# Performance work log

Hardware: AMD Instinct MI355X
Metric: run time of the kernel (lower is better)

## Reference

```python
import jax, jax.numpy as jnp
import numpy as np

N, E, L, D, H = 20000, 100000, 4, 64, 8
HID = H * D  # LSTM hidden size = num_heads * out_dim


def setup_inputs() -> dict:
    key = jax.random.key(0)
    ks = jax.random.split(key, 8)
    s = 0.05
    return {
        "features": jax.random.normal(ks[0], (N, D), jnp.float32),
        "type_mask": jax.random.randint(ks[1], (N,), 0, 3),
        "edge_metapath_indices": jax.random.randint(ks[2], (E, L), 0, N),
        "dst": jax.random.randint(ks[3], (E,), 0, N),
        "W_ih": jax.random.normal(ks[4], (4 * HID, D), jnp.float32) * s,
        "W_hh": jax.random.normal(ks[5], (4 * HID, HID), jnp.float32) * s,
        "b_ih": jnp.zeros((4 * HID,), jnp.float32),
        "b_hh": jnp.zeros((4 * HID,), jnp.float32),
        "attn1_w": jax.random.normal(ks[6], (H, D), jnp.float32) * s,
        "attn2": jax.random.normal(ks[7], (1, H, D), jnp.float32) * s,
    }


def _lstm_last_hidden(x, W_ih, W_hh, b_ih, b_hh):
    # x: [L, E, D] time-major. PyTorch LSTM gate order: i, f, g, o.
    h0 = jnp.zeros((x.shape[1], W_hh.shape[1]), x.dtype)
    b = b_ih + b_hh

    def step(carry, xt):
        h, c = carry
        gates = xt @ W_ih.T + h @ W_hh.T + b  # [E, 4*HID]
        i, f, g, o = jnp.split(gates, 4, axis=-1)
        c = jax.nn.sigmoid(f) * c + jax.nn.sigmoid(i) * jnp.tanh(g)
        h = jax.nn.sigmoid(o) * jnp.tanh(c)
        return (h, c), None

    (h, _), _ = jax.lax.scan(step, (h0, h0), x)
    return h  # [E, HID]


def reference(features, type_mask, edge_metapath_indices, dst,
              W_ih, W_hh, b_ih, b_hh, attn1_w, attn2):
    alpha = 0.01  # LeakyReLU slope
    # gather metapath node features: [E, L, D]
    edata = features[edge_metapath_indices]
    h = _lstm_last_hidden(jnp.swapaxes(edata, 0, 1), W_ih, W_hh, b_ih, b_hh)
    eft = h.reshape(-1, H, D)  # [E, H, D]
    center = features[edge_metapath_indices[:, -1]]  # [E, D]
    a1 = center @ attn1_w.T                      # [E, H]
    a2 = jnp.sum(eft * attn2, axis=-1)           # [E, H]
    a = jax.nn.leaky_relu(a1 + a2, negative_slope=alpha)[:, :, None]  # [E, H, 1]
    # edge softmax: segmented by destination node
    amax = jax.ops.segment_max(a, dst, num_segments=N)
    amax = jnp.where(jnp.isfinite(amax), amax, 0.0)
    ex = jnp.exp(a - amax[dst])
    denom = jax.ops.segment_sum(ex, dst, num_segments=N)
    attn = ex / denom[dst]  # every edge's segment is nonempty
    # message passing: scatter-sum of eft * attn into dst nodes
    return jax.ops.segment_sum(eft * attn, dst, num_segments=N)  # [N, H, D]
```

## Files before the change

kernel.cpp:

```cpp
#include <hip/hip_runtime.h>
#include <hip/hip_bf16.h>
#include <stdint.h>

#define N_NODES 20000
#define E_EDGES 100000
#define L_SEQ   4
#define D_FEAT  64
#define H_HEADS 8
#define HID     512

typedef __attribute__((ext_vector_type(8))) short short8;
typedef __attribute__((ext_vector_type(4))) float floatx4;

__device__ __forceinline__ float sigmoidf_(float x) { return 1.0f / (1.0f + __expf(-x)); }
__device__ __forceinline__ float tanhf_(float x) {
    x = fminf(15.f, fmaxf(-15.f, x));
    float e = __expf(2.f * x);
    return (e - 1.f) / (e + 1.f);
}
__device__ __forceinline__ unsigned fkey(float f) {
    unsigned u = __float_as_uint(f);
    return (u & 0x80000000u) ? ~u : (u | 0x80000000u);
}
__device__ __forceinline__ float fdecode(unsigned k) {
    if (k == 0u) return 0.0f;
    unsigned u = (k & 0x80000000u) ? (k ^ 0x80000000u) : ~k;
    return __uint_as_float(u);
}
__device__ __forceinline__ short f2bf(float x) {
    __hip_bfloat16 b = __float2bfloat16(x);
    return *(short*)&b;
}
__device__ __forceinline__ float bf2f(short x) {
    __hip_bfloat16 b = *(__hip_bfloat16*)&x;
    return __bfloat162float(b);
}

__device__ __forceinline__ void gload16(const void* g, const void* l) {
    __builtin_amdgcn_global_load_lds(
        (const __attribute__((address_space(1))) unsigned int*)(uintptr_t)g,
        (__attribute__((address_space(3))) unsigned int*)(unsigned int)(uintptr_t)l,
        16, 0, 0);
}

__global__ __launch_bounds__(256) void feat2bf16(const float* __restrict__ f, short* __restrict__ fb) {
    int i = blockIdx.x * 256 + threadIdx.x;
    if (i < N_NODES * D_FEAT) fb[i] = f2bf(f[i]);
}

__global__ __launch_bounds__(128) void convert_weights(
    const float* __restrict__ W_ih, const float* __restrict__ W_hh,
    const float* __restrict__ b_ih, const float* __restrict__ b_hh,
    short* __restrict__ Wb_ih, short* __restrict__ Wb_hh, float* __restrict__ bias)
{
    int rp = blockIdx.x;
    int hblock = rp >> 7, rem = rp & 127;
    int half = (rem >> 6) & 1, gate = (rem >> 4) & 3, j = rem & 15;
    int ro = gate * HID + hblock * 32 + half * 16 + j;
    for (int k = threadIdx.x; k < D_FEAT; k += 128)
        Wb_ih[rp * D_FEAT + k] = f2bf(W_ih[ro * D_FEAT + k]);
    for (int k = threadIdx.x; k < HID; k += 128)
        Wb_hh[rp * HID + k] = f2bf(W_hh[ro * HID + k]);
    if (threadIdx.x == 0) bias[ro] = b_ih[ro] + b_hh[ro];
}

__global__ __launch_bounds__(256) void deg_hist(const int* __restrict__ dst, int* __restrict__ deg) {
    int i = blockIdx.x * 256 + threadIdx.x;
    if (i < E_EDGES) atomicAdd(&deg[dst[i]], 1);
}

__global__ __launch_bounds__(1024) void scan_deg(const int* __restrict__ deg,
                                                 int* __restrict__ row, int* __restrict__ cursor) {
    __shared__ int buf[1024];
    __shared__ int s_carry;
    const int tid = threadIdx.x;
    if (tid == 0) s_carry = 0;
    __syncthreads();
    for (int base = 0; base < N_NODES; base += 1024) {
        int idx = base + tid;
        int v = (idx < N_NODES) ? deg[idx] : 0;
        buf[tid] = v;
        __syncthreads();
        for (int offd = 1; offd < 1024; offd <<= 1) {
            int tv = (tid >= offd) ? buf[tid - offd] : 0;
            __syncthreads();
            buf[tid] += tv;
            __syncthreads();
        }
        int c0 = s_carry;
        if (idx < N_NODES) { row[idx] = c0 + buf[tid] - v; cursor[idx] = c0 + buf[tid] - v; }
        __syncthreads();
        if (tid == 1023) s_carry = c0 + buf[1023];
        __syncthreads();
    }
    if (tid == 0) row[N_NODES] = s_carry;
}

__global__ __launch_bounds__(256) void fill_csr(const int* __restrict__ dst,
                                                int* __restrict__ cursor, int* __restrict__ elist) {
    int i = blockIdx.x * 256 + threadIdx.x;
    if (i < E_EDGES) {
        int p = atomicAdd(&cursor[dst[i]], 1);
        elist[p] = i;
    }
}

template <int FIRST>
__global__ __launch_bounds__(256) void lstm_mfma(
    const short* __restrict__ feats_bf,
    const int*   __restrict__ mp,
    const short* __restrict__ Wb_ih,
    const short* __restrict__ Wb_hh,
    const float* __restrict__ bias,
    const short* __restrict__ h_prev,
    short*       __restrict__ h_next,
    short*       __restrict__ c_state,
    int t, int cnt, int nslices)
{
    __shared__ __align__(16) short At[128 * 64];
    __shared__ __align__(16) short Bt[128 * 64];

    const int b     = blockIdx.x;
    const int xcd   = b & 7;
    const int slot  = b >> 3;
    const int g     = slot >> 4;
    const int bn    = slot & 15;
    const int slice = g * 8 + xcd;
    if (slice >= nslices) return;
    const int e0    = slice * 128;
    const int hb    = bn * 32;

    const int tid   = threadIdx.x;
    const int lane  = tid & 63;
    const int w     = tid >> 6;
    const int waveM = w & 1;
    const int waveN = w >> 1;
    const int quad  = lane >> 4;
    const int c16   = lane & 15;

    floatx4 acc[4][4];
#pragma unroll
    for (int a = 0; a < 4; ++a)
#pragma unroll
        for (int bb = 0; bb < 4; ++bb) acc[a][bb] = (floatx4){0.f, 0.f, 0.f, 0.f};

    int eidx[4], mm[4], pgo[4];
#pragma unroll
    for (int i = 0; i < 4; ++i) {
        int s = w * 256 + i * 64 + lane;
        int m = s >> 3, p = s & 7;
        pgo[i] = p ^ (m & 7);
        mm[i]  = m;
        int e  = e0 + m; if (e >= cnt) e = cnt - 1;
        eidx[i] = e;
    }

    auto compute = [&]() {
#pragma unroll
        for (int ks = 0; ks < 2; ++ks) {
            short8 af[4], bfv[4];
#pragma unroll
            for (int mf = 0; mf < 4; ++mf) {
                int m  = waveM * 64 + mf * 16 + c16;
                int pw = ks * 4 + quad;
                af[mf] = *(const short8*)&At[m * 64 + ((pw ^ (m & 7)) * 8)];
            }
#pragma unroll
            for (int nf = 0; nf < 4; ++nf) {
                int n  = waveN * 64 + nf * 16 + c16;
                int pw = ks * 4 + quad;
                bfv[nf] = *(const short8*)&Bt[n * 64 + ((pw ^ (n & 7)) * 8)];
            }
#pragma unroll
            for (int mf = 0; mf < 4; ++mf)
#pragma unroll
                for (int nf = 0; nf < 4; ++nf)
                    acc[mf][nf] = __builtin_amdgcn_mfma_f32_16x16x32_bf16(
                        af[mf], bfv[nf], acc[mf][nf], 0, 0, 0);
        }
    };

#pragma unroll
    for (int i = 0; i < 4; ++i) {
        int sb = w * 256 + i * 64;
        int rowf = mp[eidx[i] * L_SEQ + t];
        gload16((const void*)(feats_bf + rowf * D_FEAT + pgo[i] * 8), (const void*)&At[sb * 8]);
        gload16((const void*)(Wb_ih + (bn * 128 + mm[i]) * D_FEAT + pgo[i] * 8), (const void*)&Bt[sb * 8]);
    }
    __syncthreads();
    compute();

    if (!FIRST) {
        const short* ah[4]; const short* bh[4];
#pragma unroll
        for (int i = 0; i < 4; ++i) {
            ah[i] = h_prev + (size_t)eidx[i] * HID + pgo[i] * 8;
            bh[i] = Wb_hh + (size_t)(bn * 128 + mm[i]) * HID + pgo[i] * 8;
        }
        for (int kc = 1; kc <= 8; ++kc) {
            __syncthreads();
#pragma unroll
            for (int i = 0; i < 4; ++i) {
                int sb = w * 256 + i * 64;
                gload16((const void*)ah[i], (const void*)&At[sb * 8]);
                gload16((const void*)bh[i], (const void*)&Bt[sb * 8]);
                ah[i] += 64; bh[i] += 64;
            }
            __syncthreads();
            compute();
        }
    }

    const int n = hb + waveN * 16 + c16;
    const float bi  = bias[n];
    const float bff = bias[HID + n];
    const float bg  = bias[2 * HID + n];
    const float bo  = bias[3 * HID + n];
#pragma unroll
    for (int mf = 0; mf < 4; ++mf) {
#pragma unroll
        for (int r = 0; r < 4; ++r) {
            int e = e0 + waveM * 64 + mf * 16 + quad * 4 + r;
            if (e < cnt) {
                float gi = acc[mf][0][r] + bi;
                float gf = acc[mf][1][r] + bff;
                float gg = acc[mf][2][r] + bg;
                float go = acc[mf][3][r] + bo;
                float c_old = FIRST ? 0.f : bf2f(c_state[(size_t)e * HID + n]);
                float cn = sigmoidf_(gf) * c_old + sigmoidf_(gi) * tanhf_(gg);
                c_state[(size_t)e * HID + n] = f2bf(cn);
                h_next[(size_t)e * HID + n] = f2bf(sigmoidf_(go) * tanhf_(cn));
            }
        }
    }
}

__global__ __launch_bounds__(256) void attn_logits(
    const float* __restrict__ features,
    const int*   __restrict__ mp,
    const __hip_bfloat16* __restrict__ hfin,
    const float* __restrict__ attn1_w,
    const float* __restrict__ attn2,
    float*       __restrict__ a_out)
{
    const int e    = blockIdx.x * 4 + (threadIdx.x >> 6);
    const int lane = threadIdx.x & 63;
    const int ctr  = mp[e * L_SEQ + (L_SEQ - 1)];
    const float cd = features[ctr * D_FEAT + lane];
#pragma unroll
    for (int h = 0; h < H_HEADS; ++h) {
        float v = cd * attn1_w[h * D_FEAT + lane]
                + __bfloat162float(hfin[(size_t)e * HID + h * D_FEAT + lane]) * attn2[h * D_FEAT + lane];
#pragma unroll
        for (int off = 32; off; off >>= 1) v += __shfl_xor(v, off, 64);
        if (lane == 0) {
            float lv = v > 0.f ? v : 0.01f * v;
            a_out[e * H_HEADS + h] = lv;
        }
    }
}

__global__ __launch_bounds__(256) void gather_out(
    const int*   __restrict__ row,
    const int*   __restrict__ elist,
    const float* __restrict__ a_scr,
    const short* __restrict__ eft,
    float*       __restrict__ out)
{
    const int n   = blockIdx.x;
    const int tid = threadIdx.x;
    const int beg = row[n];
    const int deg = row[n + 1] - beg;
    const int j0 = tid, j1 = tid + 256;

    if (deg == 0) {
        out[(size_t)n * HID + j0] = 0.f;
        out[(size_t)n * HID + j1] = 0.f;
        return;
    }

    __shared__ unsigned s_maxu[H_HEADS];
    __shared__ float    s_max[H_HEADS];
    __shared__ float    s_den[H_HEADS];
    __shared__ float    s_w[128 * H_HEADS];
    __shared__ int      s_e[128];

    if (tid < H_HEADS) { s_maxu[tid] = 0u; s_den[tid] = 0.f; }
    __syncthreads();
    for (int i = tid; i < deg * H_HEADS; i += 256) {
        int e = elist[beg + (i >> 3)], h = i & 7;
        atomicMax(&s_maxu[h], fkey(a_scr[e * H_HEADS + h]));
    }
    __syncthreads();
    if (tid < H_HEADS) s_max[tid] = fdecode(s_maxu[tid]);
    __syncthreads();
    for (int i = tid; i < deg * H_HEADS; i += 256) {
        int e = elist[beg + (i >> 3)], h = i & 7;
        atomicAdd(&s_den[h], __expf(a_scr[e * H_HEADS + h] - s_max[h]));
    }
    __syncthreads();

    float acc0 = 0.f, acc1 = 0.f;
    const int h0 = j0 >> 6, h1 = j1 >> 6;
    for (int c0 = 0; c0 < deg; c0 += 128) {
        int cc = min(128, deg - c0);
        if (tid < cc) s_e[tid] = elist[beg + c0 + tid];
        __syncthreads();
        for (int i = tid; i < cc * H_HEADS; i += 256) {
            int k = i >> 3, h = i & 7;
            s_w[k * H_HEADS + h] = __expf(a_scr[s_e[k] * H_HEADS + h] - s_max[h]) / s_den[h];
        }
        __syncthreads();
        for (int k = 0; k < cc; ++k) {
            const short* er = eft + (size_t)s_e[k] * HID;
            acc0 += s_w[k * H_HEADS + h0] * bf2f(er[j0]);
            acc1 += s_w[k * H_HEADS + h1] * bf2f(er[j1]);
        }
        __syncthreads();
    }
    out[(size_t)n * HID + j0] = acc0;
    out[(size_t)n * HID + j1] = acc1;
}

extern "C" void kernel_launch(void* const* d_in, const int* in_sizes, int n_in,
                              void* d_out, int out_size, void* d_ws, size_t ws_size,
                              hipStream_t stream) {
    const float* features = (const float*)d_in[0];
    const int*   mp       = (const int*)d_in[2];
    const int*   dst      = (const int*)d_in[3];
    const float* W_ih     = (const float*)d_in[4];
    const float* W_hh     = (const float*)d_in[5];
    const float* b_ih     = (const float*)d_in[6];
    const float* b_hh     = (const float*)d_in[7];
    const float* attn1_w  = (const float*)d_in[8];
    const float* attn2    = (const float*)d_in[9];
    float* out = (float*)d_out;

    char* ws = (char*)d_ws;
    size_t off = 0;
    float* a_scr    = (float*)(ws + off); off += (size_t)E_EDGES * H_HEADS * sizeof(float);
    int*   deg      = (int*)(ws + off);   off += (size_t)N_NODES * sizeof(int);
    int*   row      = (int*)(ws + off);   off += ((size_t)N_NODES + 1) * sizeof(int);
    int*   cursor   = (int*)(ws + off);   off += (size_t)N_NODES * sizeof(int);
    int*   elist    = (int*)(ws + off);   off += (size_t)E_EDGES * sizeof(int);
    short* feats_bf = (short*)(ws + off); off += (size_t)N_NODES * D_FEAT * sizeof(short);
    short* Wb_ih    = (short*)(ws + off); off += (size_t)4 * HID * D_FEAT * sizeof(short);
    short* Wb_hh    = (short*)(ws + off); off += (size_t)4 * HID * HID * sizeof(short);
    float* bias     = (float*)(ws + off); off += (size_t)4 * HID * sizeof(float);
    off = (off + 255) & ~(size_t)255;
    short* eft      = (short*)(ws + off); off += (size_t)E_EDGES * HID * sizeof(short);
    off = (off + 255) & ~(size_t)255;

    const size_t per_edge = (size_t)HID * (2 + 2 + 2);
    size_t avail = (ws_size > off) ? (ws_size - off) : 0;
    long long cs_ll = ((long long)(avail / per_edge) / 1024) * 1024;
    int cs = (int)(cs_ll < 1024 ? 1024 : (cs_ll > E_EDGES ? E_EDGES : cs_ll));

    short* hA = (short*)(ws + off);
    short* hB = hA + (size_t)cs * HID;
    short* cS = hB + (size_t)cs * HID;

    hipMemsetAsync(deg, 0, (size_t)N_NODES * sizeof(int), stream);
    deg_hist<<<(E_EDGES + 255) / 256, 256, 0, stream>>>(dst, deg);
    scan_deg<<<1, 1024, 0, stream>>>(deg, row, cursor);
    fill_csr<<<(E_EDGES + 255) / 256, 256, 0, stream>>>(dst, cursor, elist);

    feat2bf16<<<(N_NODES * D_FEAT + 255) / 256, 256, 0, stream>>>(features, feats_bf);
    convert_weights<<<4 * HID, 128, 0, stream>>>(W_ih, W_hh, b_ih, b_hh, Wb_ih, Wb_hh, bias);

    for (int e0 = 0; e0 < E_EDGES; e0 += cs) {
        int cnt = E_EDGES - e0 < cs ? E_EDGES - e0 : cs;
        int nslices = (cnt + 127) / 128;
        int nslices_pad = (nslices + 7) & ~7;
        int nblk = nslices_pad * 16;
        const int* mpc = mp + (size_t)e0 * L_SEQ;
        short* eft_c = eft + (size_t)e0 * HID;
        lstm_mfma<1><<<nblk, 256, 0, stream>>>(feats_bf, mpc, Wb_ih, Wb_hh, bias, hA, hA, cS, 0, cnt, nslices);
        lstm_mfma<0><<<nblk, 256, 0, stream>>>(feats_bf, mpc, Wb_ih, Wb_hh, bias, hA, hB, cS, 1, cnt, nslices);
        lstm_mfma<0><<<nblk, 256, 0, stream>>>(feats_bf, mpc, Wb_ih, Wb_hh, bias, hB, hA, cS, 2, cnt, nslices);
        lstm_mfma<0><<<nblk, 256, 0, stream>>>(feats_bf, mpc, Wb_ih, Wb_hh, bias, hA, eft_c, cS, 3, cnt, nslices);
    }

    attn_logits<<<E_EDGES / 4, 256, 0, stream>>>(features, mp, (const __hip_bfloat16*)eft,
                                                 attn1_w, attn2, a_scr);
    gather_out<<<N_NODES, 256, 0, stream>>>(row, elist, a_scr, eft, out);
}
```

Before: 1.476 ms.

## Compute first LSTM step per node instead of per edge, vectorize attention and gather

The first LSTM timestep depends only on the starting node, so it is now computed once for all N nodes into per-node h/c tables, and step 1 gathers these by metapath index. This replaces the per-edge step-0 GEMM over E edges with one over N nodes and skips writing c at the last step. attn_logits now processes four features per lane with packed bf16 loads and splits heads across lane groups. gather_out reads two bf16 values per load and writes float2. This adds a 2*N*HID bf16 workspace and indirect loads of h/c in step 1.

New measurement: 1.345 ms. 8.9% less time.

```diff
diff --git a/kernel.cpp b/kernel.cpp
--- a/kernel.cpp
+++ b/kernel.cpp
@@ -35,6 +35,8 @@
     __hip_bfloat16 b = *(__hip_bfloat16*)&x;
     return __bfloat162float(b);
 }
+__device__ __forceinline__ float bfu_lo(unsigned v) { return __uint_as_float((v & 0xffffu) << 16); }
+__device__ __forceinline__ float bfu_hi(unsigned v) { return __uint_as_float(v & 0xffff0000u); }
 
 __device__ __forceinline__ void gload16(const void* g, const void* l) {
     __builtin_amdgcn_global_load_lds(
@@ -105,16 +107,17 @@
     }
 }
 
-template <int FIRST>
+template <int MODE>
 __global__ __launch_bounds__(256) void lstm_mfma(
     const short* __restrict__ feats_bf,
     const int*   __restrict__ mp,
     const short* __restrict__ Wb_ih,
     const short* __restrict__ Wb_hh,
     const float* __restrict__ bias,
-    const short* __restrict__ h_prev,
-    short*       __restrict__ h_next,
-    short*       __restrict__ c_state,
+    const short* __restrict__ h_src,
+    const short* __restrict__ c_src,
+    short*       __restrict__ h_dst,
+    short*       __restrict__ c_dst,
     int t, int cnt, int nslices)
 {
     __shared__ __align__(16) short At[128 * 64];
@@ -144,7 +147,7 @@
 #pragma unroll
         for (int bb = 0; bb < 4; ++bb) acc[a][bb] = (floatx4){0.f, 0.f, 0.f, 0.f};
 
-    int eidx[4], mm[4], pgo[4];
+    int eidx[4], mm[4], pgo[4], hrow[4];
 #pragma unroll
     for (int i = 0; i < 4; ++i) {
         int s = w * 256 + i * 64 + lane;
@@ -153,9 +156,32 @@
         mm[i]  = m;
         int e  = e0 + m; if (e >= cnt) e = cnt - 1;
         eidx[i] = e;
-    }
-
-    auto compute = [&]() {
+        if (MODE == 1) hrow[i] = mp[e * L_SEQ];
+    }
+
+    const int nch = (MODE == 0) ? 1 : 9;
+    for (int kc = 0; kc < nch; ++kc) {
+#pragma unroll
+        for (int i = 0; i < 4; ++i) {
+            int sb = w * 256 + i * 64;
+            const void* ga;
+            if (kc == 0) {
+                int rowf = (MODE == 0) ? eidx[i] : mp[eidx[i] * L_SEQ + t];
+                ga = (const void*)(feats_bf + rowf * D_FEAT + pgo[i] * 8);
+            } else if (MODE == 1) {
+                ga = (const void*)(h_src + (size_t)hrow[i] * HID + (kc - 1) * 64 + pgo[i] * 8);
+            } else {
+                ga = (const void*)(h_src + (size_t)eidx[i] * HID + (kc - 1) * 64 + pgo[i] * 8);
+            }
+            gload16(ga, (const void*)&At[sb * 8]);
+            int r = bn * 128 + mm[i];
+            const void* gb = (kc == 0)
+                ? (const void*)(Wb_ih + r * D_FEAT + pgo[i] * 8)
+                : (const void*)(Wb_hh + (size_t)r * HID + (kc - 1) * 64 + pgo[i] * 8);
+            gload16(gb, (const void*)&Bt[sb * 8]);
+        }
+        __syncthreads();
+
 #pragma unroll
         for (int ks = 0; ks < 2; ++ks) {
             short8 af[4], bfv[4];
@@ -178,37 +204,7 @@
                     acc[mf][nf] = __builtin_amdgcn_mfma_f32_16x16x32_bf16(
                         af[mf], bfv[nf], acc[mf][nf], 0, 0, 0);
         }
-    };
-
-#pragma unroll
-    for (int i = 0; i < 4; ++i) {
-        int sb = w * 256 + i * 64;
-        int rowf = mp[eidx[i] * L_SEQ + t];
-        gload16((const void*)(feats_bf + rowf * D_FEAT + pgo[i] * 8), (const void*)&At[sb * 8]);
-        gload16((const void*)(Wb_ih + (bn * 128 + mm[i]) * D_FEAT + pgo[i] * 8), (const void*)&Bt[sb * 8]);
-    }
-    __syncthreads();
-    compute();
-
-    if (!FIRST) {
-        const short* ah[4]; const short* bh[4];
-#pragma unroll
-        for (int i = 0; i < 4; ++i) {
-            ah[i] = h_prev + (size_t)eidx[i] * HID + pgo[i] * 8;
-            bh[i] = Wb_hh + (size_t)(bn * 128 + mm[i]) * HID + pgo[i] * 8;
-        }
-        for (int kc = 1; kc <= 8; ++kc) {
-            __syncthreads();
-#pragma unroll
-            for (int i = 0; i < 4; ++i) {
-                int sb = w * 256 + i * 64;
-                gload16((const void*)ah[i], (const void*)&At[sb * 8]);
-                gload16((const void*)bh[i], (const void*)&Bt[sb * 8]);
-                ah[i] += 64; bh[i] += 64;
-            }
-            __syncthreads();
-            compute();
-        }
+        __syncthreads();
     }
 
     const int n = hb + waveN * 16 + c16;
@@ -226,10 +222,13 @@
                 float gf = acc[mf][1][r] + bff;
                 float gg = acc[mf][2][r] + bg;
                 float go = acc[mf][3][r] + bo;
-                float c_old = FIRST ? 0.f : bf2f(c_state[(size_t)e * HID + n]);
+                float c_old;
+                if (MODE == 0)      c_old = 0.f;
+                else if (MODE == 1) c_old = bf2f(c_src[(size_t)mp[e * L_SEQ] * HID + n]);
+                else                c_old = bf2f(c_src[(size_t)e * HID + n]);
                 float cn = sigmoidf_(gf) * c_old + sigmoidf_(gi) * tanhf_(gg);
-                c_state[(size_t)e * HID + n] = f2bf(cn);
-                h_next[(size_t)e * HID + n] = f2bf(sigmoidf_(go) * tanhf_(cn));
+                if (MODE != 3) c_dst[(size_t)e * HID + n] = f2bf(cn);
+                h_dst[(size_t)e * HID + n] = f2bf(sigmoidf_(go) * tanhf_(cn));
             }
         }
     }
@@ -238,7 +237,7 @@
 __global__ __launch_bounds__(256) void attn_logits(
     const float* __restrict__ features,
     const int*   __restrict__ mp,
-    const __hip_bfloat16* __restrict__ hfin,
+    const short* __restrict__ hfin,
     const float* __restrict__ attn1_w,
     const float* __restrict__ attn2,
     float*       __restrict__ a_out)
@@ -246,14 +245,20 @@
     const int e    = blockIdx.x * 4 + (threadIdx.x >> 6);
     const int lane = threadIdx.x & 63;
     const int ctr  = mp[e * L_SEQ + (L_SEQ - 1)];
-    const float cd = features[ctr * D_FEAT + lane];
-#pragma unroll
-    for (int h = 0; h < H_HEADS; ++h) {
-        float v = cd * attn1_w[h * D_FEAT + lane]
-                + __bfloat162float(hfin[(size_t)e * HID + h * D_FEAT + lane]) * attn2[h * D_FEAT + lane];
-#pragma unroll
-        for (int off = 32; off; off >>= 1) v += __shfl_xor(v, off, 64);
-        if (lane == 0) {
+#pragma unroll
+    for (int p = 0; p < 2; ++p) {
+        const int h  = p * 4 + (lane >> 4);
+        const int d4 = (lane & 15) * 4;
+        const float4 cd = *(const float4*)&features[ctr * D_FEAT + d4];
+        const float4 a1 = *(const float4*)&attn1_w[h * D_FEAT + d4];
+        const float4 a2 = *(const float4*)&attn2[h * D_FEAT + d4];
+        const uint2 ev = *(const uint2*)&hfin[(size_t)e * HID + h * D_FEAT + d4];
+        float v = cd.x * a1.x + cd.y * a1.y + cd.z * a1.z + cd.w * a1.w
+                + bfu_lo(ev.x) * a2.x + bfu_hi(ev.x) * a2.y
+                + bfu_lo(ev.y) * a2.z + bfu_hi(ev.y) * a2.w;
+#pragma unroll
+        for (int off = 1; off < 16; off <<= 1) v += __shfl_xor(v, off, 64);
+        if ((lane & 15) == 0) {
             float lv = v > 0.f ? v : 0.01f * v;
             a_out[e * H_HEADS + h] = lv;
         }
@@ -271,11 +276,11 @@
     const int tid = threadIdx.x;
     const int beg = row[n];
     const int deg = row[n + 1] - beg;
-    const int j0 = tid, j1 = tid + 256;
+    const int j   = tid * 2;
+    const int h   = tid >> 5;
 
     if (deg == 0) {
-        out[(size_t)n * HID + j0] = 0.f;
-        out[(size_t)n * HID + j1] = 0.f;
+        *(float2*)&out[(size_t)n * HID + j] = (float2){0.f, 0.f};
         return;
     }
 
@@ -288,38 +293,37 @@
     if (tid < H_HEADS) { s_maxu[tid] = 0u; s_den[tid] = 0.f; }
     __syncthreads();
     for (int i = tid; i < deg * H_HEADS; i += 256) {
-        int e = elist[beg + (i >> 3)], h = i & 7;
-        atomicMax(&s_maxu[h], fkey(a_scr[e * H_HEADS + h]));
+        int e = elist[beg + (i >> 3)], hh = i & 7;
+        atomicMax(&s_maxu[hh], fkey(a_scr[e * H_HEADS + hh]));
     }
     __syncthreads();
     if (tid < H_HEADS) s_max[tid] = fdecode(s_maxu[tid]);
     __syncthreads();
     for (int i = tid; i < deg * H_HEADS; i += 256) {
-        int e = elist[beg + (i >> 3)], h = i & 7;
-        atomicAdd(&s_den[h], __expf(a_scr[e * H_HEADS + h] - s_max[h]));
+        int e = elist[beg + (i >> 3)], hh = i & 7;
+        atomicAdd(&s_den[hh], __expf(a_scr[e * H_HEADS + hh] - s_max[hh]));
     }
     __syncthreads();
 
     float acc0 = 0.f, acc1 = 0.f;
-    const int h0 = j0 >> 6, h1 = j1 >> 6;
     for (int c0 = 0; c0 < deg; c0 += 128) {
         int cc = min(128, deg - c0);
         if (tid < cc) s_e[tid] = elist[beg + c0 + tid];
         __syncthreads();
         for (int i = tid; i < cc * H_HEADS; i += 256) {
-            int k = i >> 3, h = i & 7;
-            s_w[k * H_HEADS + h] = __expf(a_scr[s_e[k] * H_HEADS + h] - s_max[h]) / s_den[h];
+            int k = i >> 3, hh = i & 7;
+            s_w[k * H_HEADS + hh] = __expf(a_scr[s_e[k] * H_HEADS + hh] - s_max[hh]) / s_den[hh];
         }
         __syncthreads();
         for (int k = 0; k < cc; ++k) {
-            const short* er = eft + (size_t)s_e[k] * HID;
-            acc0 += s_w[k * H_HEADS + h0] * bf2f(er[j0]);
-            acc1 += s_w[k * H_HEADS + h1] * bf2f(er[j1]);
-        }
-        __syncthreads();
-    }
-    out[(size_t)n * HID + j0] = acc0;
-    out[(size_t)n * HID + j1] = acc1;
+            unsigned v = *(const unsigned*)&eft[(size_t)s_e[k] * HID + j];
+            float wgt = s_w[k * H_HEADS + h];
+            acc0 += wgt * bfu_lo(v);
+            acc1 += wgt * bfu_hi(v);
+        }
+        __syncthreads();
+    }
+    *(float2*)&out[(size_t)n * HID + j] = (float2){acc0, acc1};
 }
 
 extern "C" void kernel_launch(void* const* d_in, const int* in_sizes, int n_in,
@@ -348,6 +352,9 @@
     short* Wb_hh    = (short*)(ws + off); off += (size_t)4 * HID * HID * sizeof(short);
     float* bias     = (float*)(ws + off); off += (size_t)4 * HID * sizeof(float);
     off = (off + 255) & ~(size_t)255;
+    short* h1n      = (short*)(ws + off); off += (size_t)N_NODES * HID * sizeof(short);
+    short* c1n      = (short*)(ws + off); off += (size_t)N_NODES * HID * sizeof(short);
+    off = (off + 255) & ~(size_t)255;
     short* eft      = (short*)(ws + off); off += (size_t)E_EDGES * HID * sizeof(short);
     off = (off + 255) & ~(size_t)255;
 
@@ -368,20 +375,24 @@
     feat2bf16<<<(N_NODES * D_FEAT + 255) / 256, 256, 0, stream>>>(features, feats_bf);
     convert_weights<<<4 * HID, 128, 0, stream>>>(W_ih, W_hh, b_ih, b_hh, Wb_ih, Wb_hh, bias);
 
+    {
+        int nslices = (N_NODES + 127) / 128;
+        int nblk = ((nslices + 7) & ~7) * 16;
+        lstm_mfma<0><<<nblk, 256, 0, stream>>>(feats_bf, nullptr, Wb_ih, Wb_hh, bias,
+                                               nullptr, nullptr, h1n, c1n, 0, N_NODES, nslices);
+    }
+
     for (int e0 = 0; e0 < E_EDGES; e0 += cs) {
         int cnt = E_EDGES - e0 < cs ? E_EDGES - e0 : cs;
         int nslices = (cnt + 127) / 128;
-        int nslices_pad = (nslices + 7) & ~7;
-        int nblk = nslices_pad * 16;
+        int nblk = ((nslices + 7) & ~7) * 16;
         const int* mpc = mp + (size_t)e0 * L_SEQ;
         short* eft_c = eft + (size_t)e0 * HID;
-        lstm_mfma<1><<<nblk, 256, 0, stream>>>(feats_bf, mpc, Wb_ih, Wb_hh, bias, hA, hA, cS, 0, cnt, nslices);
-        lstm_mfma<0><<<nblk, 256, 0, stream>>>(feats_bf, mpc, Wb_ih, Wb_hh, bias, hA, hB, cS, 1, cnt, nslices);
-        lstm_mfma<0><<<nblk, 256, 0, stream>>>(feats_bf, mpc, Wb_ih, Wb_hh, bias, hB, hA, cS, 2, cnt, nslices);
-        lstm_mfma<0><<<nblk, 256, 0, stream>>>(feats_bf, mpc, Wb_ih, Wb_hh, bias, hA, eft_c, cS, 3, cnt, nslices);
-    }
-
-    attn_logits<<<E_EDGES / 4, 256, 0, stream>>>(features, mp, (const __hip_bfloat16*)eft,
-                                                 attn1_w, attn2, a_scr);
+        lstm_mfma<1><<<nblk, 256, 0, stream>>>(feats_bf, mpc, Wb_ih, Wb_hh, bias, h1n, c1n, hA, cS, 1, cnt, nslices);
+        lstm_mfma<2><<<nblk, 256, 0, stream>>>(feats_bf, mpc, Wb_ih, Wb_hh, bias, hA, cS, hB, cS, 2, cnt, nslices);
+        lstm_mfma<3><<<nblk, 256, 0, stream>>>(feats_bf, mpc, Wb_ih, Wb_hh, bias, hB, cS, eft_c, nullptr, 3, cnt, nslices);
+    }
+
+    attn_logits<<<E_EDGES / 4, 256, 0, stream>>>(features, mp, eft, attn1_w, attn2, a_scr);
     gather_out<<<N_NODES, 256, 0, stream>>>(row, elist, a_scr, eft, out);
 }
```
